# Optimization experiments

Hardware: AMD Instinct MI355X
Metric: run time of the kernel (lower is better)

The kernel has to match this reference:

```python
import jax, jax.numpy as jnp
import numpy as np

C = 128          # input_channels == output_channels (required by residual + final conv)
MID = C // 4     # hidden width of weight/bias heads
H = W = 64
B = 4
SOFTMAX_SCALE = 1.0


def _leaky(z):
    return jnp.where(z >= 0, z, 0.2 * z)


def _conv1x1(x, w, b):
    # x: [B,Cin,H,W], w: [Cout,Cin], b: [Cout]
    return jnp.einsum('oc,bchw->bohw', w, x) + b[None, :, None, None]


def setup_inputs() -> dict:
    key = jax.random.key(0)
    ks = jax.random.split(key, 16)
    s = 0.05
    inp = {
        'x': jax.random.normal(ks[0], (B, C, H, W), dtype=jnp.float32),
        # 1x1 query / value convs
        'q_w': jax.random.normal(ks[1], (C, C), dtype=jnp.float32) * s,
        'q_b': jnp.zeros((C,), dtype=jnp.float32),
        'v_w': jax.random.normal(ks[2], (C, C), dtype=jnp.float32) * s,
        'v_b': jnp.zeros((C,), dtype=jnp.float32),
        # linear_weight head: conv1x1(C->C/4) -> leaky -> conv1x1(C/4->1)
        'lw1_w': jax.random.normal(ks[3], (MID, C), dtype=jnp.float32) * s,
        'lw1_b': jnp.zeros((MID,), dtype=jnp.float32),
        'lw2_w': jax.random.normal(ks[4], (1, MID), dtype=jnp.float32) * s,
        'lw2_b': jnp.zeros((1,), dtype=jnp.float32),
        # bias head
        'bw1_w': jax.random.normal(ks[5], (MID, C), dtype=jnp.float32) * s,
        'bw1_b': jnp.zeros((MID,), dtype=jnp.float32),
        'bw2_w': jax.random.normal(ks[6], (1, MID), dtype=jnp.float32) * s,
        'bw2_b': jnp.zeros((1,), dtype=jnp.float32),
        # final 3x3 conv (output_channels -> output_channels)
        'lin_w': jax.random.normal(ks[7], (C, C, 3, 3), dtype=jnp.float32) * s,
        'lin_b': jnp.zeros((C,), dtype=jnp.float32),
    }
    return inp


def _attn_sample(q_map, v_map, w_map, b_map):
    # q_map: [C,H,W], v_map: [C,H,W], w_map/b_map: [1,H,W]
    n = H * W
    q = q_map.reshape(C, n)                      # query tokens  [C,N]
    v = v_map.reshape(C, n)                      # value tokens  [C,N]
    w = w_map.reshape(n)
    b = b_map.reshape(n)
    # cosine-normalized keys (normalize each token over channels)
    norm = jnp.sqrt(jnp.sum(q * q, axis=0))      # [N]
    k = q / jnp.clip(norm, 1e-4)[None, :]        # [C,N]
    logits = jnp.einsum('cn,cm->nm', k, q)       # keys x queries [N,N]
    mean = jnp.mean(logits, axis=0, keepdims=True)            # [1,N]
    sparse = jax.nn.relu(logits - mean * w[None, :] + b[None, :])
    mask = (sparse != 0.0).astype(logits.dtype)
    attn = jax.nn.softmax(logits * sparse * SOFTMAX_SCALE, axis=0)
    attn = jnp.clip(attn * mask, 1e-8)
    out = jnp.einsum('cn,nm->cm', v, attn)       # [C,N]
    return out.reshape(C, H, W)


def reference(x, q_w, q_b, v_w, v_b, lw1_w, lw1_b, lw2_w, lw2_b,
              bw1_w, bw1_b, bw2_w, bw2_b, lin_w, lin_b):
    x1 = _conv1x1(x, v_w, v_b)                   # value  [B,C,H,W]
    x2 = _conv1x1(x, q_w, q_b)                   # query  [B,C,H,W]
    weight = _conv1x1(_leaky(_conv1x1(x2, lw1_w, lw1_b)), lw2_w, lw2_b)  # [B,1,H,W]
    bias = _conv1x1(_leaky(_conv1x1(x2, bw1_w, bw1_b)), bw2_w, bw2_b)    # [B,1,H,W]
    y = jax.vmap(_attn_sample)(x2, x1, weight, bias)                      # [B,C,H,W]
    y = jax.lax.conv_general_dilated(
        y, lin_w, window_strides=(1, 1), padding='SAME',
        dimension_numbers=('NCHW', 'OIHW', 'NCHW'))
    y = _leaky(y + lin_b[None, :, None, None])
    return y + x
```

## Files before the change

### kernel.cpp

```cpp
#include <hip/hip_runtime.h>
#include <math.h>

#define BB 4
#define CC 128
#define NN 4096
#define HH 64
#define WW 64
#define YTP 4356

typedef __attribute__((ext_vector_type(8))) short bf16x8;
typedef __attribute__((ext_vector_type(4))) float f32x4;

__device__ inline unsigned short f2bf(float f) {
  unsigned int u = __float_as_uint(f);
  unsigned int r = (u + 0x7FFFu + ((u >> 16) & 1u)) >> 16;
  return (unsigned short)r;
}
__device__ inline float bf2f(short s) {
  union { unsigned u; float f; } x;
  x.u = ((unsigned)(unsigned short)s) << 16;
  return x.f;
}

__global__ __launch_bounds__(256) void xt_kernel(
    const float* __restrict__ x, unsigned short* __restrict__ xtb) {
  int b = blockIdx.y;
  int n0 = blockIdx.x * 64;
  int t = threadIdx.x;
  __shared__ float xs[CC][65];
  for (int l = 0; l < 32; l++) {
    int idx = t + 256 * l;
    int px = idx & 63, c = idx >> 6;
    xs[c][px] = x[((size_t)b * CC + c) * NN + n0 + px];
  }
  __syncthreads();
  int n = t & 63, ch = t >> 6;
  unsigned o[16];
#pragma unroll
  for (int i = 0; i < 32; i += 2) {
    o[i >> 1] = (unsigned)f2bf(xs[32 * ch + i][n]) |
                ((unsigned)f2bf(xs[32 * ch + i + 1][n]) << 16);
  }
  unsigned short* dst = xtb + ((size_t)b * NN + n0 + n) * CC + 32 * ch;
#pragma unroll
  for (int k = 0; k < 4; k++) {
    uint4 v; v.x = o[4 * k]; v.y = o[4 * k + 1]; v.z = o[4 * k + 2]; v.w = o[4 * k + 3];
    *(uint4*)(dst + 8 * k) = v;
  }
}

__global__ __launch_bounds__(256) void wrepack_kernel(
    const float* __restrict__ qw, const float* __restrict__ vw,
    const float* __restrict__ lw1w, const float* __restrict__ bw1w,
    const float* __restrict__ lw, unsigned short* __restrict__ qwb,
    unsigned short* __restrict__ vwb, unsigned short* __restrict__ hwb,
    unsigned short* __restrict__ Wt) {
  int idx = blockIdx.x * 256 + threadIdx.x;
  if (idx < 16384) { qwb[idx] = f2bf(qw[idx]); return; }
  idx -= 16384;
  if (idx < 16384) { vwb[idx] = f2bf(vw[idx]); return; }
  idx -= 16384;
  if (idx < 4096) { hwb[idx] = f2bf(lw1w[idx]); return; }
  idx -= 4096;
  if (idx < 4096) { hwb[4096 + idx] = f2bf(bw1w[idx]); return; }
  idx -= 4096;
  if (idx < CC * 1152) {
    int co = idx / 1152, rem = idx % 1152;
    int tap = rem >> 7, ci = rem & 127;
    Wt[idx] = f2bf(lw[(size_t)(co * CC + ci) * 9 + tap]);
  }
}

__global__ __launch_bounds__(256) void qv_mfma(
    const unsigned short* __restrict__ xtb, const unsigned short* __restrict__ qwb,
    const unsigned short* __restrict__ vwb, const unsigned short* __restrict__ hwb,
    const float* __restrict__ qb, const float* __restrict__ vb,
    const float* __restrict__ lw1b, const float* __restrict__ lw2w,
    const float* __restrict__ lw2b, const float* __restrict__ bw1b,
    const float* __restrict__ bw2w, const float* __restrict__ bw2b,
    unsigned short* __restrict__ qt, unsigned short* __restrict__ qtn,
    float* __restrict__ nrm, float* __restrict__ pSkey,
    unsigned short* __restrict__ vbuf, float* __restrict__ pSumV,
    float* __restrict__ wmap, float* __restrict__ bmap) {
  int b = blockIdx.y;
  int nb = blockIdx.x;
  int n0 = nb * 64;
  int t = threadIdx.x, w = t >> 6, lane = t & 63;
  int col = lane & 15, oct = lane >> 4;
  __shared__ float qs[4][16][132];
  __shared__ float partK[4][128];
  __shared__ float partV[4][128];
  const unsigned short* xb = xtb + (size_t)b * NN * CC;

  f32x4 aq[8], av[8];
#pragma unroll
  for (int i = 0; i < 8; i++) { aq[i] = (f32x4)0.f; av[i] = (f32x4)0.f; }
#pragma unroll
  for (int kc = 0; kc < 4; kc++) {
    bf16x8 Xf = *(const bf16x8*)(xb + (size_t)(n0 + 16 * w + col) * CC + kc * 32 + oct * 8);
#pragma unroll
    for (int ct = 0; ct < 8; ct++) {
      bf16x8 Qf = *(const bf16x8*)(qwb + (16 * ct + col) * CC + kc * 32 + oct * 8);
      aq[ct] = __builtin_amdgcn_mfma_f32_16x16x32_bf16(Xf, Qf, aq[ct], 0, 0, 0);
      bf16x8 Vf = *(const bf16x8*)(vwb + (16 * ct + col) * CC + kc * 32 + oct * 8);
      av[ct] = __builtin_amdgcn_mfma_f32_16x16x32_bf16(Vf, Xf, av[ct], 0, 0, 0);
    }
  }

  unsigned short* vbb = vbuf + (size_t)b * CC * NN;
#pragma unroll
  for (int ct = 0; ct < 8; ct++) {
#pragma unroll
    for (int r = 0; r < 4; r++) {
      int c = 16 * ct + 4 * oct + r;
      float val = av[ct][r] + vb[c];
      vbb[(size_t)c * NN + n0 + 16 * w + col] = f2bf(val);
      float sv = val;
      sv += __shfl_xor(sv, 1); sv += __shfl_xor(sv, 2);
      sv += __shfl_xor(sv, 4); sv += __shfl_xor(sv, 8);
      if (col == 0) partV[w][c] = sv;
    }
  }

#pragma unroll
  for (int ct = 0; ct < 8; ct++) {
#pragma unroll
    for (int r = 0; r < 4; r++) {
      int c = 16 * ct + col;
      qs[w][4 * oct + r][c] = aq[ct][r] + qb[c];
    }
  }
  int row = lane >> 2, cq = (lane & 3) * 32;
  float vals[32];
  float ssq = 0.f;
#pragma unroll
  for (int i = 0; i < 32; i += 4) {
    float4 v4 = *(const float4*)&qs[w][row][cq + i];
    vals[i] = v4.x; vals[i + 1] = v4.y; vals[i + 2] = v4.z; vals[i + 3] = v4.w;
    ssq += v4.x * v4.x + v4.y * v4.y + v4.z * v4.z + v4.w * v4.w;
  }
  ssq += __shfl_xor(ssq, 1); ssq += __shfl_xor(ssq, 2);
  float nm = fmaxf(sqrtf(ssq), 1e-4f), sc = 1.0f / nm;
  int gp = b * NN + n0 + 16 * w + row;
  if ((lane & 3) == 0) nrm[gp] = nm;
  unsigned outq[16], outn[16];
  float sk[32];
#pragma unroll
  for (int i = 0; i < 32; i += 2) {
    unsigned short u0 = f2bf(vals[i]), u1 = f2bf(vals[i + 1]);
    unsigned short m0 = f2bf(vals[i] * sc), m1 = f2bf(vals[i + 1] * sc);
    outq[i >> 1] = (unsigned)u0 | ((unsigned)u1 << 16);
    outn[i >> 1] = (unsigned)m0 | ((unsigned)m1 << 16);
    sk[i] = bf2f((short)m0); sk[i + 1] = bf2f((short)m1);
  }
  unsigned short* qtp = qt + (size_t)gp * CC + cq;
  unsigned short* qnp = qtn + (size_t)gp * CC + cq;
#pragma unroll
  for (int k = 0; k < 4; k++) {
    uint4 v; v.x = outq[4 * k]; v.y = outq[4 * k + 1]; v.z = outq[4 * k + 2]; v.w = outq[4 * k + 3];
    *(uint4*)(qtp + 8 * k) = v;
    uint4 u; u.x = outn[4 * k]; u.y = outn[4 * k + 1]; u.z = outn[4 * k + 2]; u.w = outn[4 * k + 3];
    *(uint4*)(qnp + 8 * k) = u;
  }
#pragma unroll
  for (int i = 0; i < 32; i++) {
    float v = sk[i];
    v += __shfl_xor(v, 4); v += __shfl_xor(v, 8);
    v += __shfl_xor(v, 16); v += __shfl_xor(v, 32);
    if ((lane >> 2) == 0) partK[w][cq + i] = v;
  }

  f32x4 ah[4];
#pragma unroll
  for (int i = 0; i < 4; i++) ah[i] = (f32x4)0.f;
#pragma unroll
  for (int kc = 0; kc < 4; kc++) {
    float4 a0 = *(const float4*)&qs[w][col][kc * 32 + oct * 8];
    float4 a1 = *(const float4*)&qs[w][col][kc * 32 + oct * 8 + 4];
    union { unsigned short s[8]; bf16x8 v; } af;
    af.s[0] = f2bf(a0.x); af.s[1] = f2bf(a0.y); af.s[2] = f2bf(a0.z); af.s[3] = f2bf(a0.w);
    af.s[4] = f2bf(a1.x); af.s[5] = f2bf(a1.y); af.s[6] = f2bf(a1.z); af.s[7] = f2bf(a1.w);
#pragma unroll
    for (int ct = 0; ct < 4; ct++) {
      bf16x8 Bf = *(const bf16x8*)(hwb + (16 * ct + col) * CC + kc * 32 + oct * 8);
      ah[ct] = __builtin_amdgcn_mfma_f32_16x16x32_bf16(af.v, Bf, ah[ct], 0, 0, 0);
    }
  }
  float b1l[2], b1b[2], w2l[2], w2b[2];
#pragma unroll
  for (int ct = 0; ct < 2; ct++) {
    int mid = 16 * ct + col;
    b1l[ct] = lw1b[mid]; w2l[ct] = lw2w[mid];
    b1b[ct] = bw1b[mid]; w2b[ct] = bw2w[mid];
  }
#pragma unroll
  for (int r = 0; r < 4; r++) {
    float wp = 0.f, bp = 0.f;
#pragma unroll
    for (int ct = 0; ct < 2; ct++) {
      float zl = ah[ct][r] + b1l[ct];
      zl = (zl >= 0.f) ? zl : 0.2f * zl;
      wp += w2l[ct] * zl;
      float zb = ah[ct + 2][r] + b1b[ct];
      zb = (zb >= 0.f) ? zb : 0.2f * zb;
      bp += w2b[ct] * zb;
    }
    wp += __shfl_xor(wp, 1); wp += __shfl_xor(wp, 2);
    wp += __shfl_xor(wp, 4); wp += __shfl_xor(wp, 8);
    bp += __shfl_xor(bp, 1); bp += __shfl_xor(bp, 2);
    bp += __shfl_xor(bp, 4); bp += __shfl_xor(bp, 8);
    if (col == 0) {
      int g = b * NN + n0 + 16 * w + 4 * oct + r;
      wmap[g] = wp + lw2b[0];
      bmap[g] = bp + bw2b[0];
    }
  }

  __syncthreads();
  int blk = b * 64 + nb;
  if (t < 128) {
    float s = (partK[0][t] + partK[1][t]) + (partK[2][t] + partK[3][t]);
    pSkey[(size_t)blk * 128 + t] = s;
  } else {
    int c = t - 128;
    float s = (partV[0][c] + partV[1][c]) + (partV[2][c] + partV[3][c]);
    pSumV[(size_t)blk * 128 + c] = s;
  }
}

__global__ __launch_bounds__(256) void reduce_kernel(
    const float* __restrict__ pSkey, const float* __restrict__ pSumV,
    float* __restrict__ Skey, float* __restrict__ SumV) {
  int b = blockIdx.x;
  int t = threadIdx.x;
  const float* src = (t < 128) ? pSkey : pSumV;
  int c = t & 127;
  float s = 0.f;
#pragma unroll 8
  for (int nb = 0; nb < 64; nb++)
    s += src[((size_t)b * 64 + nb) * 128 + c];
  if (t < 128) Skey[b * CC + c] = s;
  else SumV[b * CC + c] = s;
}

__global__ __launch_bounds__(256) void stats_kernel(
    const unsigned short* __restrict__ qtn, const float* __restrict__ Skey,
    const float* __restrict__ nrm, const float* __restrict__ wmap,
    const float* __restrict__ bmap, float* __restrict__ c1a,
    float* __restrict__ zda) {
  int g = blockIdx.x * 256 + threadIdx.x;
  int b = g >> 12;
  __shared__ float sk[CC];
  if (threadIdx.x < CC) sk[threadIdx.x] = Skey[b * CC + threadIdx.x];
  __syncthreads();
  const unsigned short* qp = qtn + (size_t)g * CC;
  float dot = 0.f;
#pragma unroll
  for (int i = 0; i < CC; i += 8) {
    bf16x8 v = *(const bf16x8*)(qp + i);
    dot += bf2f(v[0]) * sk[i]     + bf2f(v[1]) * sk[i + 1]
         + bf2f(v[2]) * sk[i + 2] + bf2f(v[3]) * sk[i + 3]
         + bf2f(v[4]) * sk[i + 4] + bf2f(v[5]) * sk[i + 5]
         + bf2f(v[6]) * sk[i + 6] + bf2f(v[7]) * sk[i + 7];
  }
  float c1 = dot * (1.0f / NN) * wmap[g] - bmap[g];
  float nm = nrm[g];
  c1a[g] = c1;
  zda[g] = nm * fmaxf(nm - c1, 0.f);
}

__global__ __launch_bounds__(256, 2) void qk_sparse(
    const unsigned short* __restrict__ qt, const unsigned short* __restrict__ qtn,
    const float* __restrict__ c1a, const float* __restrict__ zda,
    float* __restrict__ Zacc, const unsigned short* __restrict__ vb16,
    float* __restrict__ Ypart, int* __restrict__ flags) {
  int lin = blockIdx.x;
  int mtile = lin >> 6;
  int bks = lin & 63;
  int b = bks >> 4, ks = bks & 15;
  int t = threadIdx.x, wave = t >> 6, lane = t & 63;
  int col = lane & 15, oct = lane >> 4;
  int m0 = mtile * 128 + 32 * wave;
  int bucket = b * 128 + (m0 >> 5);

  __shared__ unsigned short Bt[8][4096];
  __shared__ __align__(16) unsigned short tS[4][32][40];

  const unsigned short* qtb  = qt  + (size_t)b * NN * CC;
  const unsigned short* qtnb = qtn + (size_t)b * NN * CC;
  const unsigned short* vbb  = vb16 + (size_t)b * CC * NN;

  bf16x8 A[2][4];
#pragma unroll
  for (int mt = 0; mt < 2; mt++)
#pragma unroll
    for (int kc = 0; kc < 4; kc++)
      A[mt][kc] = *(const bf16x8*)(qtb + (size_t)(m0 + 16 * mt + col) * CC + 32 * kc + 8 * oct);

  float stc1[2][4], stzd[2][4];
#pragma unroll
  for (int mt = 0; mt < 2; mt++) {
    int m = m0 + 16 * mt + col;
    float c1 = c1a[(size_t)b * NN + m];
    float zd = zda[(size_t)b * NN + m];
#pragma unroll
    for (int r = 0; r < 4; r++) {
      stc1[mt][r] = __shfl(c1, 4 * oct + r);
      stzd[mt][r] = __shfl(zd, 4 * oct + r);
    }
  }

  int n0base = ks * 256;
  {
    int f0 = wave, f1 = wave + 4;
    size_t off0 = (size_t)(16 * (f0 >> 2) + col) * CC + (4 * (f0 & 3) + oct) * 8;
    size_t off1 = (size_t)(16 * (f1 >> 2) + col) * CC + (4 * (f1 & 3) + oct) * 8;
#pragma unroll
    for (int it = 0; it < 8; it++) {
      size_t nb0 = (size_t)(n0base + it * 32) * CC;
      uint4 r0 = *(const uint4*)(qtnb + nb0 + off0);
      uint4 r1 = *(const uint4*)(qtnb + nb0 + off1);
      *(uint4*)&Bt[it][f0 * 512 + lane * 8] = r0;
      *(uint4*)&Bt[it][f1 * 512 + lane * 8] = r1;
    }
  }
  __syncthreads();

  float zp[2][4];
#pragma unroll
  for (int mt = 0; mt < 2; mt++)
#pragma unroll
    for (int r = 0; r < 4; r++) zp[mt][r] = 0.f;
  f32x4 pvacc[2][8];
#pragma unroll
  for (int mt = 0; mt < 2; mt++)
#pragma unroll
    for (int ct = 0; ct < 8; ct++) pvacc[mt][ct] = (f32x4)0.f;
  bool didwork = false;

  for (int it = 0; it < 8; it++) {
    f32x4 acc[2][2];
    acc[0][0] = (f32x4)0.f; acc[0][1] = (f32x4)0.f;
    acc[1][0] = (f32x4)0.f; acc[1][1] = (f32x4)0.f;
#pragma unroll
    for (int nt = 0; nt < 2; nt++)
#pragma unroll
      for (int kc = 0; kc < 4; kc++) {
        bf16x8 Bf = *(const bf16x8*)&Bt[it][(nt * 4 + kc) * 512 + lane * 8];
        acc[0][nt] = __builtin_amdgcn_mfma_f32_16x16x32_bf16(A[0][kc], Bf, acc[0][nt], 0, 0, 0);
        acc[1][nt] = __builtin_amdgcn_mfma_f32_16x16x32_bf16(A[1][kc], Bf, acc[1][nt], 0, 0, 0);
      }
    float fm = -1e30f;
#pragma unroll
    for (int mt = 0; mt < 2; mt++)
#pragma unroll
      for (int r = 0; r < 4; r++) {
        float lm = fmaxf(acc[mt][0][r], acc[mt][1][r]);
        float ub = fmaxf(lm * fmaxf(lm - stc1[mt][r], 0.f), 0.f);
        fm = fmaxf(fm, ub - stzd[mt][r]);
      }
    if (__any(fm > -18.4207f)) {
      didwork = true;
      int n0 = n0base + it * 32;
#pragma unroll
      for (int mt = 0; mt < 2; mt++)
#pragma unroll
        for (int nt = 0; nt < 2; nt++)
#pragma unroll
          for (int r = 0; r < 4; r++) {
            float l = acc[mt][nt][r];
            float s = l - stc1[mt][r];
            float z = l * fmaxf(s, 0.f);
            float e = __expf(z - stzd[mt][r]);
            zp[mt][r] += e;
            tS[wave][16 * mt + 4 * oct + r][16 * nt + col] = f2bf((s > 0.f) ? e : 0.f);
          }
      bf16x8 Pa = *(const bf16x8*)&tS[wave][col][8 * oct];
      bf16x8 Pb = *(const bf16x8*)&tS[wave][16 + col][8 * oct];
#pragma unroll
      for (int ct = 0; ct < 8; ct++) {
        bf16x8 Vf = *(const bf16x8*)(vbb + (size_t)(16 * ct + col) * NN + n0 + 8 * oct);
        pvacc[0][ct] = __builtin_amdgcn_mfma_f32_16x16x32_bf16(Vf, Pa, pvacc[0][ct], 0, 0, 0);
        pvacc[1][ct] = __builtin_amdgcn_mfma_f32_16x16x32_bf16(Vf, Pb, pvacc[1][ct], 0, 0, 0);
      }
    }
  }

  if (didwork) {
#pragma unroll
    for (int mt = 0; mt < 2; mt++)
#pragma unroll
      for (int r = 0; r < 4; r++) {
        float v = zp[mt][r];
        v += __shfl_xor(v, 1); v += __shfl_xor(v, 2);
        v += __shfl_xor(v, 4); v += __shfl_xor(v, 8);
        if (col == 0)
          atomicAdd(Zacc + (size_t)b * NN + m0 + 16 * mt + 4 * oct + r, v);
      }
    float* yp = Ypart + ((size_t)bucket * 16 + ks) * (32 * CC);
#pragma unroll
    for (int mt = 0; mt < 2; mt++)
#pragma unroll
      for (int ct = 0; ct < 8; ct++) {
        float4 o;
        o.x = pvacc[mt][ct][0]; o.y = pvacc[mt][ct][1];
        o.z = pvacc[mt][ct][2]; o.w = pvacc[mt][ct][3];
        *(float4*)(yp + (16 * mt + col) * CC + 16 * ct + 4 * oct) = o;
      }
    if (lane == 0) flags[bucket * 16 + ks] = 1;
  }
}

__global__ __launch_bounds__(256) void yfin_kernel(
    const float* __restrict__ Ypart, const int* __restrict__ flags,
    const float* __restrict__ Zacc, const float* __restrict__ SumV,
    unsigned short* __restrict__ Yt) {
  int bucket = blockIdx.x;
  int b = bucket >> 7;
  int m0 = (bucket & 127) * 32;
  int t = threadIdx.x;
  int mi = t >> 3, c0 = (t & 7) * 16;
  int m = m0 + mi;
  __shared__ int fl[16];
  if (t < 16) fl[t] = flags[bucket * 16 + t];
  __syncthreads();
  float rZ = 1.0f / Zacc[(size_t)b * NN + m];
  int h = m >> 6, ww = m & 63;
  const float* yb = Ypart + (size_t)bucket * 16 * (32 * CC) + mi * CC + c0;
  const float* sv = SumV + b * CC + c0;
  unsigned short* yp = Yt + ((size_t)b * YTP + (size_t)(h + 1) * 66 + (ww + 1)) * CC + c0;
  float a[16];
#pragma unroll
  for (int j = 0; j < 16; j++) a[j] = 0.f;
  for (int ks = 0; ks < 16; ks++) {
    if (!fl[ks]) continue;
    const float* ya = yb + (size_t)ks * (32 * CC);
#pragma unroll
    for (int j = 0; j < 4; j++) {
      float4 v = *(const float4*)(ya + 4 * j);
      a[4 * j] += v.x; a[4 * j + 1] += v.y; a[4 * j + 2] += v.z; a[4 * j + 3] += v.w;
    }
  }
  unsigned ov[8];
#pragma unroll
  for (int j = 0; j < 8; j++) {
    float2 s = *(const float2*)(sv + 2 * j);
    float y0 = a[2 * j] * rZ + 1e-8f * s.x;
    float y1 = a[2 * j + 1] * rZ + 1e-8f * s.y;
    ov[j] = (unsigned)f2bf(y0) | ((unsigned)f2bf(y1) << 16);
  }
  uint4 o0; o0.x = ov[0]; o0.y = ov[1]; o0.z = ov[2]; o0.w = ov[3];
  uint4 o1; o1.x = ov[4]; o1.y = ov[5]; o1.z = ov[6]; o1.w = ov[7];
  *(uint4*)yp = o0;
  *(uint4*)(yp + 8) = o1;
}

__global__ __launch_bounds__(256, 4) void conv_mfma(
    const unsigned short* __restrict__ Yt, const unsigned short* __restrict__ Wt,
    const float* __restrict__ x, const float* __restrict__ lb,
    float* __restrict__ out) {
  int h = blockIdx.x;
  int by = blockIdx.y;
  int b = blockIdx.z;
  int t = threadIdx.x;
  int wave = t >> 6, lane = t & 63;
  int col = lane & 15, oct = lane >> 4;
  int w0 = by * 16;
  __shared__ __align__(16) unsigned short ys[54 * 128];

  const unsigned short* Yb = Yt + (size_t)b * YTP * CC;
  for (int e = t; e < 864; e += 256) {
    int row = e >> 4;
    int c16 = e & 15;
    int dr = row / 18, j = row - dr * 18;
    uint4 v = *(const uint4*)(Yb + ((size_t)(h + dr) * 66 + w0 + j) * CC + c16 * 8);
    int slot = row * 16 + (c16 ^ (row & 7));
    *(uint4*)(ys + slot * 8) = v;
  }
  __syncthreads();

  f32x4 acc[2];
  acc[0] = (f32x4)0.f; acc[1] = (f32x4)0.f;

#pragma unroll
  for (int tap = 0; tap < 9; tap++) {
    int dr = tap / 3, dc = tap % 3;
    int arow = dr * 18 + dc + col;
#pragma unroll
    for (int kc = 0; kc < 4; kc++) {
      int slot = arow * 16 + ((kc * 4 + oct) ^ (arow & 7));
      bf16x8 Af = *(const bf16x8*)(ys + slot * 8);
#pragma unroll
      for (int ct = 0; ct < 2; ct++) {
        bf16x8 Bf = *(const bf16x8*)(Wt +
            (size_t)(32 * wave + 16 * ct + col) * 1152 + tap * 128 + 32 * kc + 8 * oct);
        acc[ct] = __builtin_amdgcn_mfma_f32_16x16x32_bf16(Af, Bf, acc[ct], 0, 0, 0);
      }
    }
  }
#pragma unroll
  for (int ct = 0; ct < 2; ct++) {
    int co = 32 * wave + 16 * ct + col;
    float bv = lb[co];
    int n = h * 64 + w0 + 4 * oct;
    size_t base = ((size_t)b * CC + co) * NN + n;
    float4 xi = *(const float4*)(x + base);
    float4 o;
    float z0 = acc[ct][0] + bv; o.x = ((z0 >= 0.f) ? z0 : 0.2f * z0) + xi.x;
    float z1 = acc[ct][1] + bv; o.y = ((z1 >= 0.f) ? z1 : 0.2f * z1) + xi.y;
    float z2 = acc[ct][2] + bv; o.z = ((z2 >= 0.f) ? z2 : 0.2f * z2) + xi.z;
    float z3 = acc[ct][3] + bv; o.w = ((z3 >= 0.f) ? z3 : 0.2f * z3) + xi.w;
    *(float4*)(out + base) = o;
  }
}

extern "C" void kernel_launch(void* const* d_in, const int* in_sizes, int n_in,
                              void* d_out, int out_size, void* d_ws, size_t ws_size,
                              hipStream_t stream) {
  const float* x    = (const float*)d_in[0];
  const float* q_w  = (const float*)d_in[1];
  const float* q_b  = (const float*)d_in[2];
  const float* v_w  = (const float*)d_in[3];
  const float* v_b  = (const float*)d_in[4];
  const float* lw1w = (const float*)d_in[5];
  const float* lw1b = (const float*)d_in[6];
  const float* lw2w = (const float*)d_in[7];
  const float* lw2b = (const float*)d_in[8];
  const float* bw1w = (const float*)d_in[9];
  const float* bw1b = (const float*)d_in[10];
  const float* bw2w = (const float*)d_in[11];
  const float* bw2b = (const float*)d_in[12];
  const float* linw = (const float*)d_in[13];
  const float* linb = (const float*)d_in[14];
  float* out = (float*)d_out;

  const size_t BCN = (size_t)BB * CC * NN;
  const size_t BN  = (size_t)BB * NN;

  unsigned short* xtb = (unsigned short*)d_ws;
  unsigned short* qt  = xtb + BCN;
  unsigned short* qtn = qt + BCN;
  unsigned short* vb16 = qtn + BCN;
  unsigned short* Yt  = vb16 + BCN;
  unsigned short* qwb = Yt + (size_t)BB * YTP * CC;
  unsigned short* vwb = qwb + CC * CC;
  unsigned short* hwb = vwb + CC * CC;
  unsigned short* Wt  = hwb + 64 * CC;
  float* nrmb = (float*)(Wt + (size_t)CC * 1152);
  float* wmap = nrmb + BN;
  float* bmap = wmap + BN;
  float* SumV = bmap + BN;
  float* Skey = SumV + (size_t)BB * CC;
  float* c1a  = Skey + (size_t)BB * CC;
  float* zda  = c1a + BN;
  float* Zacc = zda + BN;
  int*   flags = (int*)(Zacc + BN);
  float* pSkey = (float*)(flags + 512 * 16);
  float* pSumV = pSkey + 256 * 128;
  float* Ypart = pSumV + 256 * 128;

  size_t zbytes = BN * sizeof(float) + 512 * 16 * sizeof(int);
  hipMemsetAsync(Zacc, 0, zbytes, stream);
  hipMemsetAsync(Yt, 0, (size_t)BB * YTP * CC * sizeof(unsigned short), stream);

  hipLaunchKernelGGL(xt_kernel, dim3(NN / 64, BB), dim3(256), 0, stream, x, xtb);
  hipLaunchKernelGGL(wrepack_kernel, dim3((188416 + 255) / 256), dim3(256), 0,
                     stream, q_w, v_w, lw1w, bw1w, linw, qwb, vwb, hwb, Wt);
  hipLaunchKernelGGL(qv_mfma, dim3(NN / 64, BB), dim3(256), 0, stream,
                     xtb, qwb, vwb, hwb, q_b, v_b, lw1b, lw2w, lw2b,
                     bw1b, bw2w, bw2b, qt, qtn, nrmb, pSkey, vb16, pSumV,
                     wmap, bmap);
  hipLaunchKernelGGL(reduce_kernel, dim3(BB), dim3(256), 0, stream,
                     pSkey, pSumV, Skey, SumV);
  hipLaunchKernelGGL(stats_kernel, dim3(BN / 256), dim3(256), 0, stream,
                     qtn, Skey, nrmb, wmap, bmap, c1a, zda);
  hipLaunchKernelGGL(qk_sparse, dim3(2048), dim3(256), 0, stream,
                     qt, qtn, c1a, zda, Zacc, vb16, Ypart, flags);
  hipLaunchKernelGGL(yfin_kernel, dim3(512), dim3(256), 0, stream,
                     Ypart, flags, Zacc, SumV, Yt);
  hipLaunchKernelGGL(conv_mfma, dim3(HH, 4, BB), dim3(256), 0, stream,
                     Yt, Wt, x, linb, out);
}
```

Measured before the change: 212.4 us.

## Split qv_mfma waves into separate query and value roles over smaller tiles

Each block now covers 32 tokens instead of 64. Its four waves are paired: one wave of each pair computes the value projection and the other computes the query projection with normalization and the weight/bias heads. This halves per-wave accumulator registers and doubles the grid, aiming for higher occupancy and more parallelism in the projection stage. In exchange the partial-sum buffers and the reduce kernel loop double in size, the X fragment is loaded by two waves, and the query waves do more work than the value waves.

```diff
diff --git a/kernel.cpp b/kernel.cpp
--- a/kernel.cpp
+++ b/kernel.cpp
@@ -84,146 +84,158 @@
     float* __restrict__ wmap, float* __restrict__ bmap) {
   int b = blockIdx.y;
   int nb = blockIdx.x;
-  int n0 = nb * 64;
   int t = threadIdx.x, w = t >> 6, lane = t & 63;
+  int role = w & 1, pg = w >> 1;
+  int n0 = nb * 32 + pg * 16;
   int col = lane & 15, oct = lane >> 4;
-  __shared__ float qs[4][16][132];
-  __shared__ float partK[4][128];
-  __shared__ float partV[4][128];
+  __shared__ float qs[2][16][132];
+  __shared__ float partK[2][128];
+  __shared__ float partV[2][128];
   const unsigned short* xb = xtb + (size_t)b * NN * CC;
 
-  f32x4 aq[8], av[8];
-#pragma unroll
-  for (int i = 0; i < 8; i++) { aq[i] = (f32x4)0.f; av[i] = (f32x4)0.f; }
-#pragma unroll
-  for (int kc = 0; kc < 4; kc++) {
-    bf16x8 Xf = *(const bf16x8*)(xb + (size_t)(n0 + 16 * w + col) * CC + kc * 32 + oct * 8);
+  if (role == 1) {
+    f32x4 av[8];
+#pragma unroll
+    for (int i = 0; i < 8; i++) av[i] = (f32x4)0.f;
+#pragma unroll
+    for (int kc = 0; kc < 4; kc++) {
+      bf16x8 Xf = *(const bf16x8*)(xb + (size_t)(n0 + col) * CC + kc * 32 + oct * 8);
+#pragma unroll
+      for (int ct = 0; ct < 8; ct++) {
+        bf16x8 Vf = *(const bf16x8*)(vwb + (16 * ct + col) * CC + kc * 32 + oct * 8);
+        av[ct] = __builtin_amdgcn_mfma_f32_16x16x32_bf16(Vf, Xf, av[ct], 0, 0, 0);
+      }
+    }
+    unsigned short* vbb = vbuf + (size_t)b * CC * NN;
 #pragma unroll
     for (int ct = 0; ct < 8; ct++) {
-      bf16x8 Qf = *(const bf16x8*)(qwb + (16 * ct + col) * CC + kc * 32 + oct * 8);
-      aq[ct] = __builtin_amdgcn_mfma_f32_16x16x32_bf16(Xf, Qf, aq[ct], 0, 0, 0);
-      bf16x8 Vf = *(const bf16x8*)(vwb + (16 * ct + col) * CC + kc * 32 + oct * 8);
-      av[ct] = __builtin_amdgcn_mfma_f32_16x16x32_bf16(Vf, Xf, av[ct], 0, 0, 0);
-    }
-  }
-
-  unsigned short* vbb = vbuf + (size_t)b * CC * NN;
-#pragma unroll
-  for (int ct = 0; ct < 8; ct++) {
+#pragma unroll
+      for (int r = 0; r < 4; r++) {
+        int c = 16 * ct + 4 * oct + r;
+        float val = av[ct][r] + vb[c];
+        vbb[(size_t)c * NN + n0 + col] = f2bf(val);
+        float sv = val;
+        sv += __shfl_xor(sv, 1); sv += __shfl_xor(sv, 2);
+        sv += __shfl_xor(sv, 4); sv += __shfl_xor(sv, 8);
+        if (col == 0) partV[pg][c] = sv;
+      }
+    }
+  } else {
+    f32x4 aq[8];
+#pragma unroll
+    for (int i = 0; i < 8; i++) aq[i] = (f32x4)0.f;
+#pragma unroll
+    for (int kc = 0; kc < 4; kc++) {
+      bf16x8 Xf = *(const bf16x8*)(xb + (size_t)(n0 + col) * CC + kc * 32 + oct * 8);
+#pragma unroll
+      for (int ct = 0; ct < 8; ct++) {
+        bf16x8 Qf = *(const bf16x8*)(qwb + (16 * ct + col) * CC + kc * 32 + oct * 8);
+        aq[ct] = __builtin_amdgcn_mfma_f32_16x16x32_bf16(Xf, Qf, aq[ct], 0, 0, 0);
+      }
+    }
+#pragma unroll
+    for (int ct = 0; ct < 8; ct++) {
+#pragma unroll
+      for (int r = 0; r < 4; r++) {
+        int c = 16 * ct + col;
+        qs[pg][4 * oct + r][c] = aq[ct][r] + qb[c];
+      }
+    }
+    int row = lane >> 2, cq = (lane & 3) * 32;
+    float vals[32];
+    float ssq = 0.f;
+#pragma unroll
+    for (int i = 0; i < 32; i += 4) {
+      float4 v4 = *(const float4*)&qs[pg][row][cq + i];
+      vals[i] = v4.x; vals[i + 1] = v4.y; vals[i + 2] = v4.z; vals[i + 3] = v4.w;
+      ssq += v4.x * v4.x + v4.y * v4.y + v4.z * v4.z + v4.w * v4.w;
+    }
+    ssq += __shfl_xor(ssq, 1); ssq += __shfl_xor(ssq, 2);
+    float nm = fmaxf(sqrtf(ssq), 1e-4f), sc = 1.0f / nm;
+    int gp = b * NN + n0 + row;
+    if ((lane & 3) == 0) nrm[gp] = nm;
+    unsigned outq[16], outn[16];
+    float sk[32];
+#pragma unroll
+    for (int i = 0; i < 32; i += 2) {
+      unsigned short u0 = f2bf(vals[i]), u1 = f2bf(vals[i + 1]);
+      unsigned short m0 = f2bf(vals[i] * sc), m1 = f2bf(vals[i + 1] * sc);
+      outq[i >> 1] = (unsigned)u0 | ((unsigned)u1 << 16);
+      outn[i >> 1] = (unsigned)m0 | ((unsigned)m1 << 16);
+      sk[i] = bf2f((short)m0); sk[i + 1] = bf2f((short)m1);
+    }
+    unsigned short* qtp = qt + (size_t)gp * CC + cq;
+    unsigned short* qnp = qtn + (size_t)gp * CC + cq;
+#pragma unroll
+    for (int k = 0; k < 4; k++) {
+      uint4 v; v.x = outq[4 * k]; v.y = outq[4 * k + 1]; v.z = outq[4 * k + 2]; v.w = outq[4 * k + 3];
+      *(uint4*)(qtp + 8 * k) = v;
+      uint4 u; u.x = outn[4 * k]; u.y = outn[4 * k + 1]; u.z = outn[4 * k + 2]; u.w = outn[4 * k + 3];
+      *(uint4*)(qnp + 8 * k) = u;
+    }
+#pragma unroll
+    for (int i = 0; i < 32; i++) {
+      float v = sk[i];
+      v += __shfl_xor(v, 4); v += __shfl_xor(v, 8);
+      v += __shfl_xor(v, 16); v += __shfl_xor(v, 32);
+      if ((lane >> 2) == 0) partK[pg][cq + i] = v;
+    }
+
+    f32x4 ah[4];
+#pragma unroll
+    for (int i = 0; i < 4; i++) ah[i] = (f32x4)0.f;
+#pragma unroll
+    for (int kc = 0; kc < 4; kc++) {
+      float4 a0 = *(const float4*)&qs[pg][col][kc * 32 + oct * 8];
+      float4 a1 = *(const float4*)&qs[pg][col][kc * 32 + oct * 8 + 4];
+      union { unsigned short s[8]; bf16x8 v; } af;
+      af.s[0] = f2bf(a0.x); af.s[1] = f2bf(a0.y); af.s[2] = f2bf(a0.z); af.s[3] = f2bf(a0.w);
+      af.s[4] = f2bf(a1.x); af.s[5] = f2bf(a1.y); af.s[6] = f2bf(a1.z); af.s[7] = f2bf(a1.w);
+#pragma unroll
+      for (int ct = 0; ct < 4; ct++) {
+        bf16x8 Bf = *(const bf16x8*)(hwb + (16 * ct + col) * CC + kc * 32 + oct * 8);
+        ah[ct] = __builtin_amdgcn_mfma_f32_16x16x32_bf16(af.v, Bf, ah[ct], 0, 0, 0);
+      }
+    }
+    float b1l[2], b1b[2], w2l[2], w2b[2];
+#pragma unroll
+    for (int ct = 0; ct < 2; ct++) {
+      int mid = 16 * ct + col;
+      b1l[ct] = lw1b[mid]; w2l[ct] = lw2w[mid];
+      b1b[ct] = bw1b[mid]; w2b[ct] = bw2w[mid];
+    }
 #pragma unroll
     for (int r = 0; r < 4; r++) {
-      int c = 16 * ct + 4 * oct + r;
-      float val = av[ct][r] + vb[c];
-      vbb[(size_t)c * NN + n0 + 16 * w + col] = f2bf(val);
-      float sv = val;
-      sv += __shfl_xor(sv, 1); sv += __shfl_xor(sv, 2);
-      sv += __shfl_xor(sv, 4); sv += __shfl_xor(sv, 8);
-      if (col == 0) partV[w][c] = sv;
-    }
-  }
-
-#pragma unroll
-  for (int ct = 0; ct < 8; ct++) {
-#pragma unroll
-    for (int r = 0; r < 4; r++) {
-      int c = 16 * ct + col;
-      qs[w][4 * oct + r][c] = aq[ct][r] + qb[c];
-    }
-  }
-  int row = lane >> 2, cq = (lane & 3) * 32;
-  float vals[32];
-  float ssq = 0.f;
-#pragma unroll
-  for (int i = 0; i < 32; i += 4) {
-    float4 v4 = *(const float4*)&qs[w][row][cq + i];
-    vals[i] = v4.x; vals[i + 1] = v4.y; vals[i + 2] = v4.z; vals[i + 3] = v4.w;
-    ssq += v4.x * v4.x + v4.y * v4.y + v4.z * v4.z + v4.w * v4.w;
-  }
-  ssq += __shfl_xor(ssq, 1); ssq += __shfl_xor(ssq, 2);
-  float nm = fmaxf(sqrtf(ssq), 1e-4f), sc = 1.0f / nm;
-  int gp = b * NN + n0 + 16 * w + row;
-  if ((lane & 3) == 0) nrm[gp] = nm;
-  unsigned outq[16], outn[16];
-  float sk[32];
-#pragma unroll
-  for (int i = 0; i < 32; i += 2) {
-    unsigned short u0 = f2bf(vals[i]), u1 = f2bf(vals[i + 1]);
-    unsigned short m0 = f2bf(vals[i] * sc), m1 = f2bf(vals[i + 1] * sc);
-    outq[i >> 1] = (unsigned)u0 | ((unsigned)u1 << 16);
-    outn[i >> 1] = (unsigned)m0 | ((unsigned)m1 << 16);
-    sk[i] = bf2f((short)m0); sk[i + 1] = bf2f((short)m1);
-  }
-  unsigned short* qtp = qt + (size_t)gp * CC + cq;
-  unsigned short* qnp = qtn + (size_t)gp * CC + cq;
-#pragma unroll
-  for (int k = 0; k < 4; k++) {
-    uint4 v; v.x = outq[4 * k]; v.y = outq[4 * k + 1]; v.z = outq[4 * k + 2]; v.w = outq[4 * k + 3];
-    *(uint4*)(qtp + 8 * k) = v;
-    uint4 u; u.x = outn[4 * k]; u.y = outn[4 * k + 1]; u.z = outn[4 * k + 2]; u.w = outn[4 * k + 3];
-    *(uint4*)(qnp + 8 * k) = u;
-  }
-#pragma unroll
-  for (int i = 0; i < 32; i++) {
-    float v = sk[i];
-    v += __shfl_xor(v, 4); v += __shfl_xor(v, 8);
-    v += __shfl_xor(v, 16); v += __shfl_xor(v, 32);
-    if ((lane >> 2) == 0) partK[w][cq + i] = v;
-  }
-
-  f32x4 ah[4];
-#pragma unroll
-  for (int i = 0; i < 4; i++) ah[i] = (f32x4)0.f;
-#pragma unroll
-  for (int kc = 0; kc < 4; kc++) {
-    float4 a0 = *(const float4*)&qs[w][col][kc * 32 + oct * 8];
-    float4 a1 = *(const float4*)&qs[w][col][kc * 32 + oct * 8 + 4];
-    union { unsigned short s[8]; bf16x8 v; } af;
-    af.s[0] = f2bf(a0.x); af.s[1] = f2bf(a0.y); af.s[2] = f2bf(a0.z); af.s[3] = f2bf(a0.w);
-    af.s[4] = f2bf(a1.x); af.s[5] = f2bf(a1.y); af.s[6] = f2bf(a1.z); af.s[7] = f2bf(a1.w);
-#pragma unroll
-    for (int ct = 0; ct < 4; ct++) {
-      bf16x8 Bf = *(const bf16x8*)(hwb + (16 * ct + col) * CC + kc * 32 + oct * 8);
-      ah[ct] = __builtin_amdgcn_mfma_f32_16x16x32_bf16(af.v, Bf, ah[ct], 0, 0, 0);
-    }
-  }
-  float b1l[2], b1b[2], w2l[2], w2b[2];
-#pragma unroll
-  for (int ct = 0; ct < 2; ct++) {
-    int mid = 16 * ct + col;
-    b1l[ct] = lw1b[mid]; w2l[ct] = lw2w[mid];
-    b1b[ct] = bw1b[mid]; w2b[ct] = bw2w[mid];
-  }
-#pragma unroll
-  for (int r = 0; r < 4; r++) {
-    float wp = 0.f, bp = 0.f;
-#pragma unroll
-    for (int ct = 0; ct < 2; ct++) {
-      float zl = ah[ct][r] + b1l[ct];
-      zl = (zl >= 0.f) ? zl : 0.2f * zl;
-      wp += w2l[ct] * zl;
-      float zb = ah[ct + 2][r] + b1b[ct];
-      zb = (zb >= 0.f) ? zb : 0.2f * zb;
-      bp += w2b[ct] * zb;
-    }
-    wp += __shfl_xor(wp, 1); wp += __shfl_xor(wp, 2);
-    wp += __shfl_xor(wp, 4); wp += __shfl_xor(wp, 8);
-    bp += __shfl_xor(bp, 1); bp += __shfl_xor(bp, 2);
-    bp += __shfl_xor(bp, 4); bp += __shfl_xor(bp, 8);
-    if (col == 0) {
-      int g = b * NN + n0 + 16 * w + 4 * oct + r;
-      wmap[g] = wp + lw2b[0];
-      bmap[g] = bp + bw2b[0];
+      float wp = 0.f, bp = 0.f;
+#pragma unroll
+      for (int ct = 0; ct < 2; ct++) {
+        float zl = ah[ct][r] + b1l[ct];
+        zl = (zl >= 0.f) ? zl : 0.2f * zl;
+        wp += w2l[ct] * zl;
+        float zb = ah[ct + 2][r] + b1b[ct];
+        zb = (zb >= 0.f) ? zb : 0.2f * zb;
+        bp += w2b[ct] * zb;
+      }
+      wp += __shfl_xor(wp, 1); wp += __shfl_xor(wp, 2);
+      wp += __shfl_xor(wp, 4); wp += __shfl_xor(wp, 8);
+      bp += __shfl_xor(bp, 1); bp += __shfl_xor(bp, 2);
+      bp += __shfl_xor(bp, 4); bp += __shfl_xor(bp, 8);
+      if (col == 0) {
+        int g = b * NN + n0 + 4 * oct + r;
+        wmap[g] = wp + lw2b[0];
+        bmap[g] = bp + bw2b[0];
+      }
     }
   }
 
   __syncthreads();
-  int blk = b * 64 + nb;
+  int blk = b * 128 + nb;
   if (t < 128) {
-    float s = (partK[0][t] + partK[1][t]) + (partK[2][t] + partK[3][t]);
+    float s = partK[0][t] + partK[1][t];
     pSkey[(size_t)blk * 128 + t] = s;
   } else {
     int c = t - 128;
-    float s = (partV[0][c] + partV[1][c]) + (partV[2][c] + partV[3][c]);
+    float s = partV[0][c] + partV[1][c];
     pSumV[(size_t)blk * 128 + c] = s;
   }
 }
@@ -237,8 +249,8 @@
   int c = t & 127;
   float s = 0.f;
 #pragma unroll 8
-  for (int nb = 0; nb < 64; nb++)
-    s += src[((size_t)b * 64 + nb) * 128 + c];
+  for (int nb = 0; nb < 128; nb++)
+    s += src[((size_t)b * 128 + nb) * 128 + c];
   if (t < 128) Skey[b * CC + c] = s;
   else SumV[b * CC + c] = s;
 }
@@ -556,8 +568,8 @@
   float* Zacc = zda + BN;
   int*   flags = (int*)(Zacc + BN);
   float* pSkey = (float*)(flags + 512 * 16);
-  float* pSumV = pSkey + 256 * 128;
-  float* Ypart = pSumV + 256 * 128;
+  float* pSumV = pSkey + 512 * 128;
+  float* Ypart = pSumV + 512 * 128;
 
   size_t zbytes = BN * sizeof(float) + 512 * 16 * sizeof(int);
   hipMemsetAsync(Zacc, 0, zbytes, stream);
@@ -566,7 +578,7 @@
   hipLaunchKernelGGL(xt_kernel, dim3(NN / 64, BB), dim3(256), 0, stream, x, xtb);
   hipLaunchKernelGGL(wrepack_kernel, dim3((188416 + 255) / 256), dim3(256), 0,
                      stream, q_w, v_w, lw1w, bw1w, linw, qwb, vwb, hwb, Wt);
-  hipLaunchKernelGGL(qv_mfma, dim3(NN / 64, BB), dim3(256), 0, stream,
+  hipLaunchKernelGGL(qv_mfma, dim3(NN / 32, BB), dim3(256), 0, stream,
                      xtb, qwb, vwb, hwb, q_b, v_b, lw1b, lw2w, lw2b,
                      bw1b, bw2w, bw2b, qt, qtn, nrmb, pSkey, vb16, pSumV,
                      wmap, bmap);
```

After: 208.6 us. No clear change (-1.8%).
